# Kernel tuning notes

Hardware: AMD Instinct MI355X
Metric: run time of the kernel (lower is better)

## Reference

```python
import jax, jax.numpy as jnp
import numpy as np

K = 5          # kernel_size
BETA = 15.0    # soft-max temperature
PAD = (K - 1) // 2  # fixed_padding with dilation=1: pad_beg = pad_end = 2


def setup_inputs() -> dict:
    key = jax.random.key(0)
    kx, kw = jax.random.split(key)
    x = jax.random.normal(kx, (16, 8, 256, 256), dtype=jnp.float32)
    weight = jax.random.normal(kw, (8, 8, K, K), dtype=jnp.float32) * 0.1
    return {"x": x, "weight": weight}


def reference(x, weight):
    """Morphological dilation2d with soft-max (logsumexp) reduction.

    Equivalent to: unfold(pad(x)) -> (B,1,C*K*K,L); add weight.view(O,-1);
    logsumexp(beta * .) / beta over the C*K*K axis; reshape to (B,O,H,W).
    Implemented as a streaming logsumexp over the K*K taps to avoid the
    huge unfold intermediate.
    """
    B, C, H, W = x.shape
    O = weight.shape[0]
    xp = jnp.pad(x, ((0, 0), (0, 0), (PAD, PAD), (PAD, PAD)))
    acc = None
    for ki in range(K):
        for kj in range(K):
            xs = xp[:, :, ki:ki + H, kj:kj + W]              # (B,C,H,W)
            w_tap = weight[:, :, ki, kj]                      # (O,C)
            # beta * (w + x), broadcast to (B,O,C,H,W)
            t = BETA * (xs[:, None, :, :, :] + w_tap[None, :, :, None, None])
            lse = jax.nn.logsumexp(t, axis=2)                 # (B,O,H,W)
            acc = lse if acc is None else jnp.logaddexp(acc, lse)
    return acc / BETA
```

## Files before the change

### kernel.cpp

```cpp
#include <hip/hip_runtime.h>
#include <hip/hip_bf16.h>
#include <math.h>

#define KW 5
#define BETA 15.0f
#define MSHIFT 3.0f
#define CIN 8
#define COUT 8
#define HH 256
#define WW 256
#define TWW 16
#define TWH 8
#define WCW 20
#define WCH 12
#define WSLOTS (WCW * WCH)
#define NG 8

typedef float f32x4 __attribute__((ext_vector_type(4)));
typedef short s16x8 __attribute__((ext_vector_type(8)));

static __device__ __forceinline__ unsigned f2bf(float f) {
    unsigned u = __float_as_uint(f);
    return (u + 0x7FFFu + ((u >> 16) & 1u)) >> 16;
}

__global__ void build_afrag(const float* __restrict__ wgt,
                            s16x8* __restrict__ table) {
    int i = blockIdx.x * 64 + threadIdx.x;
    int g = i >> 6, lane = i & 63;
    int quad = lane >> 4, row = lane & 15;
    int tap30 = g * 4 + quad;
    int tr = tap30 / KW, tc = tap30 % KW;
    s16x8 af;
    #pragma unroll
    for (int j = 0; j < CIN; ++j) {
        float v = 0.0f;
        if (tap30 < 30) {
            if (row < COUT) {
                if (tr <= 4)
                    v = __expf(BETA * wgt[(row * CIN + j) * (KW * KW) + tr * KW + tc]);
            } else {
                if (tr >= 1)
                    v = __expf(BETA * wgt[((row - 8) * CIN + j) * (KW * KW) + (tr - 1) * KW + tc]);
            }
        }
        af[j] = (short)f2bf(v);
    }
    table[i] = af;
}

__global__ __launch_bounds__(256, 5) void morph_mfma(
    const float* __restrict__ x, const s16x8* __restrict__ table,
    float* __restrict__ out)
{
    __shared__ int4 exs[4 * WSLOTS];

    const int tid  = threadIdx.x;
    const int lane = tid & 63;
    const int wv   = tid >> 6;
    const int px   = lane & 15;
    const int quad = lane >> 4;

    const int lid = blockIdx.x;
    const int sw  = (lid & 7) * 256 + (lid >> 3);
    const int b   = sw >> 7;
    const int t   = sw & 127;
    const int h0  = (t >> 2) * TWH;
    const int w0  = (t & 3) * 64 + wv * TWW;

    int4* myex = &exs[wv * WSLOTS];

    s16x8 afrag[NG];
    int   toff[NG];
    #pragma unroll
    for (int g = 0; g < NG; ++g) {
        afrag[g] = table[g * 64 + lane];
        int tap30 = g * 4 + quad;
        int tcl   = tap30 < 30 ? tap30 : 29;
        toff[g] = (tcl / KW) * WCW + (tcl % KW);
    }

    for (int s = lane; s < WSLOTS; s += 64) {
        int r = s / WCW, col = s - r * WCW;
        int gh = h0 + r - 2, gw = w0 + col - 2;
        bool ok = ((unsigned)gh < (unsigned)HH) & ((unsigned)gw < (unsigned)WW);
        unsigned pk[4];
        #pragma unroll
        for (int c2 = 0; c2 < 4; ++c2) {
            float v0 = 0.0f, v1 = 0.0f;
            if (ok) {
                v0 = x[((b * CIN + 2 * c2) * HH + gh) * WW + gw];
                v1 = x[((b * CIN + 2 * c2 + 1) * HH + gh) * WW + gw];
            }
            float2 e = make_float2(
                __builtin_amdgcn_exp2f(fmaf(v0, 21.6404256f, -64.9212768f)),
                __builtin_amdgcn_exp2f(fmaf(v1, 21.6404256f, -64.9212768f)));
            __hip_bfloat162 h2 = __float22bfloat162_rn(e);
            pk[c2] = *reinterpret_cast<unsigned*>(&h2);
        }
        int4 p; p.x = pk[0]; p.y = pk[1]; p.z = pk[2]; p.w = pk[3];
        myex[s] = p;
    }

    const int dh = quad >> 1;
    const int ob = (quad & 1) * 4;
    const float LN2B = 0.04620981f;
    #pragma unroll
    for (int hp = 0; hp < 4; ++hp) {
        const int base = (2 * hp) * WCW + px;
        f32x4 acc0 = {0.0f, 0.0f, 0.0f, 0.0f};
        f32x4 acc1 = {0.0f, 0.0f, 0.0f, 0.0f};
        #pragma unroll
        for (int g = 0; g < NG; ++g) {
            s16x8 bfr = *(const s16x8*)&myex[base + toff[g]];
            if (g & 1)
                acc1 = __builtin_amdgcn_mfma_f32_16x16x32_bf16(
                           afrag[g], bfr, acc1, 0, 0, 0);
            else
                acc0 = __builtin_amdgcn_mfma_f32_16x16x32_bf16(
                           afrag[g], bfr, acc0, 0, 0, 0);
        }
        const int h = h0 + 2 * hp + dh;
        #pragma unroll
        for (int r = 0; r < 4; ++r) {
            float s = acc0[r] + acc1[r];
            out[((b * COUT + ob + r) * HH + h) * WW + w0 + px]
                = fmaf(__builtin_amdgcn_logf(s), LN2B, MSHIFT);
        }
    }
}

extern "C" void kernel_launch(void* const* d_in, const int* in_sizes, int n_in,
                              void* d_out, int out_size, void* d_ws, size_t ws_size,
                              hipStream_t stream) {
    const float* x   = (const float*)d_in[0];
    const float* wgt = (const float*)d_in[1];
    float* out  = (float*)d_out;
    s16x8* tab  = (s16x8*)d_ws;

    const int B = in_sizes[0] / (CIN * HH * WW);
    const int nblk = B * (HH / TWH) * (WW / 64);
    build_afrag<<<NG, 64, 0, stream>>>(wgt, tab);
    morph_mfma<<<nblk, 256, 0, stream>>>(x, tab, out);
}
```

Measured before the change: 94.89 us.

## Precompute padded exp(x) bf16 image in global memory, read it directly in MFMA kernel

Moves the exp/bf16 packing of the input halo out of the MFMA kernel into a separate pass that writes a padded, channel-packed exp image (260x260 per batch) to workspace. The MFMA kernel then reads B fragments straight from global memory instead of staging them through LDS, which removes the redundant halo recomputation and the shared-memory staging. In exchange it adds an extra kernel launch and a full write plus reread of the expanded image (16 bytes per pixel), and the global reads rely on cache hits for the overlapping taps. The occupancy hint is raised from 5 to 6.

```diff
diff --git a/kernel.cpp b/kernel.cpp
--- a/kernel.cpp
+++ b/kernel.cpp
@@ -9,12 +9,12 @@
 #define COUT 8
 #define HH 256
 #define WW 256
-#define TWW 16
+#define EXH 260
+#define EXW 260
+#define EXPIX (EXH * EXW)
+#define PB 265
+#define NG 8
 #define TWH 8
-#define WCW 20
-#define WCH 12
-#define WSLOTS (WCW * WCH)
-#define NG 8
 
 typedef float f32x4 __attribute__((ext_vector_type(4)));
 typedef short s16x8 __attribute__((ext_vector_type(8)));
@@ -49,12 +49,40 @@
     table[i] = af;
 }
 
-__global__ __launch_bounds__(256, 5) void morph_mfma(
-    const float* __restrict__ x, const s16x8* __restrict__ table,
+__global__ __launch_bounds__(256) void build_ex(
+    const float* __restrict__ x, s16x8* __restrict__ ex)
+{
+    const int lid = blockIdx.x;
+    const int sw  = (lid & 7) * 530 + (lid >> 3);
+    const int b   = sw / PB;
+    const int xb  = sw - b * PB;
+    const int p   = xb * 256 + threadIdx.x;
+    if (p >= EXPIX) return;
+    const int r   = p / EXW, col = p - r * EXW;
+    const int gh = r - 2, gw = col - 2;
+    const bool ok = ((unsigned)gh < (unsigned)HH) & ((unsigned)gw < (unsigned)WW);
+    unsigned pk[4];
+    #pragma unroll
+    for (int c2 = 0; c2 < 4; ++c2) {
+        float v0 = 0.0f, v1 = 0.0f;
+        if (ok) {
+            v0 = x[((b * CIN + 2 * c2) * HH + gh) * WW + gw];
+            v1 = x[((b * CIN + 2 * c2 + 1) * HH + gh) * WW + gw];
+        }
+        float2 e = make_float2(
+            __builtin_amdgcn_exp2f(fmaf(v0, 21.6404256f, -64.9212768f)),
+            __builtin_amdgcn_exp2f(fmaf(v1, 21.6404256f, -64.9212768f)));
+        __hip_bfloat162 h2 = __float22bfloat162_rn(e);
+        pk[c2] = *reinterpret_cast<unsigned*>(&h2);
+    }
+    int4 q; q.x = pk[0]; q.y = pk[1]; q.z = pk[2]; q.w = pk[3];
+    *reinterpret_cast<int4*>(&ex[b * EXPIX + p]) = q;
+}
+
+__global__ __launch_bounds__(256, 6) void morph_mfma(
+    const s16x8* __restrict__ ex, const s16x8* __restrict__ table,
     float* __restrict__ out)
 {
-    __shared__ int4 exs[4 * WSLOTS];
-
     const int tid  = threadIdx.x;
     const int lane = tid & 63;
     const int wv   = tid >> 6;
@@ -66,9 +94,7 @@
     const int b   = sw >> 7;
     const int t   = sw & 127;
     const int h0  = (t >> 2) * TWH;
-    const int w0  = (t & 3) * 64 + wv * TWW;
-
-    int4* myex = &exs[wv * WSLOTS];
+    const int w0  = (t & 3) * 64 + wv * 16;
 
     s16x8 afrag[NG];
     int   toff[NG];
@@ -77,42 +103,23 @@
         afrag[g] = table[g * 64 + lane];
         int tap30 = g * 4 + quad;
         int tcl   = tap30 < 30 ? tap30 : 29;
-        toff[g] = (tcl / KW) * WCW + (tcl % KW);
+        toff[g] = (tcl / KW) * EXW + (tcl % KW);
     }
 
-    for (int s = lane; s < WSLOTS; s += 64) {
-        int r = s / WCW, col = s - r * WCW;
-        int gh = h0 + r - 2, gw = w0 + col - 2;
-        bool ok = ((unsigned)gh < (unsigned)HH) & ((unsigned)gw < (unsigned)WW);
-        unsigned pk[4];
-        #pragma unroll
-        for (int c2 = 0; c2 < 4; ++c2) {
-            float v0 = 0.0f, v1 = 0.0f;
-            if (ok) {
-                v0 = x[((b * CIN + 2 * c2) * HH + gh) * WW + gw];
-                v1 = x[((b * CIN + 2 * c2 + 1) * HH + gh) * WW + gw];
-            }
-            float2 e = make_float2(
-                __builtin_amdgcn_exp2f(fmaf(v0, 21.6404256f, -64.9212768f)),
-                __builtin_amdgcn_exp2f(fmaf(v1, 21.6404256f, -64.9212768f)));
-            __hip_bfloat162 h2 = __float22bfloat162_rn(e);
-            pk[c2] = *reinterpret_cast<unsigned*>(&h2);
-        }
-        int4 p; p.x = pk[0]; p.y = pk[1]; p.z = pk[2]; p.w = pk[3];
-        myex[s] = p;
-    }
+    const s16x8* exb = ex + b * EXPIX;
+    const int base0 = h0 * EXW + w0 + px;
 
     const int dh = quad >> 1;
     const int ob = (quad & 1) * 4;
     const float LN2B = 0.04620981f;
     #pragma unroll
     for (int hp = 0; hp < 4; ++hp) {
-        const int base = (2 * hp) * WCW + px;
+        const int rp = base0 + 2 * hp * EXW;
         f32x4 acc0 = {0.0f, 0.0f, 0.0f, 0.0f};
         f32x4 acc1 = {0.0f, 0.0f, 0.0f, 0.0f};
         #pragma unroll
         for (int g = 0; g < NG; ++g) {
-            s16x8 bfr = *(const s16x8*)&myex[base + toff[g]];
+            s16x8 bfr = exb[rp + toff[g]];
             if (g & 1)
                 acc1 = __builtin_amdgcn_mfma_f32_16x16x32_bf16(
                            afrag[g], bfr, acc1, 0, 0, 0);
@@ -137,9 +144,11 @@
     const float* wgt = (const float*)d_in[1];
     float* out  = (float*)d_out;
     s16x8* tab  = (s16x8*)d_ws;
+    s16x8* ex   = (s16x8*)((char*)d_ws + 8192);
 
     const int B = in_sizes[0] / (CIN * HH * WW);
+    build_afrag<<<NG, 64, 0, stream>>>(wgt, tab);
+    build_ex<<<8 * 530, 256, 0, stream>>>(x, ex);
     const int nblk = B * (HH / TWH) * (WW / 64);
-    build_afrag<<<NG, 64, 0, stream>>>(wgt, tab);
-    morph_mfma<<<nblk, 256, 0, stream>>>(x, tab, out);
+    morph_mfma<<<nblk, 256, 0, stream>>>(ex, tab, out);
 }
```

Result: slower. 104.9 us (+10.5%).
